# Kernel tuning notes

Measured on AMD Instinct MI355X. Metric: run time of the kernel, lower is better.

Reference implementation:

```python
import jax, jax.numpy as jnp
import numpy as np

D = 1024  # input_dim


def setup_inputs() -> dict:
    key = jax.random.key(0)
    ks = jax.random.split(key, 7)
    scale = 1.0 / np.sqrt(D)
    x = jax.random.normal(ks[0], (4, D, 2048), dtype=jnp.float32)
    Wq = jax.random.uniform(ks[1], (D, D), jnp.float32, -scale, scale)
    bq = jax.random.uniform(ks[2], (D,), jnp.float32, -scale, scale)
    Wk = jax.random.uniform(ks[3], (D, D), jnp.float32, -scale, scale)
    bk = jax.random.uniform(ks[4], (D,), jnp.float32, -scale, scale)
    Wv = jax.random.uniform(ks[5], (D, D), jnp.float32, -scale, scale)
    bv = jax.random.uniform(ks[6], (D,), jnp.float32, -scale, scale)
    return {"x": x, "Wq": Wq, "bq": bq, "Wk": Wk, "bk": bk, "Wv": Wv, "bv": bv}


def reference(x, Wq, bq, Wk, bk, Wv, bv):
    # x: [B, D, S] -> [B, S, D]
    xt = jnp.transpose(x, (0, 2, 1))
    # torch nn.Linear: y = x @ W^T + b
    q = jnp.einsum('bsd,ed->bse', xt, Wq) + bq
    k = jnp.einsum('bsd,ed->bse', xt, Wk) + bk
    v = jnp.einsum('bsd,ed->bse', xt, Wv) + bv
    scores = jnp.einsum('bse,bte->bst', q, k) / jnp.sqrt(jnp.float32(D))
    attn = jax.nn.softmax(scores, axis=2)
    out = jnp.einsum('bst,bte->bse', attn, v)  # [B, S, D]
    return out
```

## Files before the change

### kernel.cpp

```cpp
#include <hip/hip_runtime.h>
#include <stdint.h>

typedef unsigned short us16;
typedef unsigned short us8  __attribute__((ext_vector_type(8)));
typedef unsigned short us4v __attribute__((ext_vector_type(4)));
typedef __bf16         bf16x8 __attribute__((ext_vector_type(8)));
typedef float          f32x4  __attribute__((ext_vector_type(4)));

__device__ __forceinline__ us16 f2bf(float f) {
    union { float f; unsigned int u; } c; c.f = f;
    unsigned int u = (c.u + 0x7fffu + ((c.u >> 16) & 1u)) >> 16;
    return (us16)u;
}

__device__ __forceinline__ void async16(const us16* g, us16* l) {
    __builtin_amdgcn_global_load_lds(
        (const __attribute__((address_space(1))) unsigned int*)g,
        (__attribute__((address_space(3))) unsigned int*)l,
        16, 0, 0);
}

template <int N> __device__ __forceinline__ void wait_vm() {
    if constexpr (N == 8)      asm volatile("s_waitcnt vmcnt(8)" ::: "memory");
    else if constexpr (N == 6) asm volatile("s_waitcnt vmcnt(6)" ::: "memory");
    else if constexpr (N == 4) asm volatile("s_waitcnt vmcnt(4)" ::: "memory");
    else if constexpr (N == 3) asm volatile("s_waitcnt vmcnt(3)" ::: "memory");
    else                       asm volatile("s_waitcnt vmcnt(0)" ::: "memory");
}

template <int EPI, int MI, int NJ>
__device__ __forceinline__ void gemm_pipe(
        const us16* __restrict__ A, const us16* __restrict__ B,
        void* __restrict__ C, const float* __restrict__ bias,
        float* __restrict__ L,
        int M, int K, int x, int y, us16* lds) {
    constexpr int BM  = 32 * MI;
    constexpr int BN  = 64 * NJ;
    constexpr int IA  = BM / 128;
    constexpr int IB  = BN / 128;
    constexpr int EA  = BM * 32;
    constexpr int BUF = EA + BN * 32;
    constexpr int LD  = IA + IB;

    const int tid  = threadIdx.x;
    const int lane = tid & 63, wid = tid >> 6;
    const int l15  = lane & 15, quad = lane >> 4;
    const int wm   = wid >> 2, wn = wid & 3;
    const int m0   = x * BM, n0 = y * BN;

    const int gc8  = (((lane & 3) ^ ((lane >> 2) & 3) ^ ((lane >> 4) & 3))) * 8;
    const int lsub = lane >> 2;

    const us16* Ag[IA]; int Al[IA];
#pragma unroll
    for (int c = 0; c < IA; c++) {
        const int r = wid * (16 * IA) + c * 16;
        Ag[c] = A + (size_t)(m0 + r + lsub) * K + gc8;
        Al[c] = r * 32;
    }
    const us16* Bg[IB]; int Bl[IB];
#pragma unroll
    for (int c = 0; c < IB; c++) {
        const int r = wid * (16 * IB) + c * 16;
        Bg[c] = B + (size_t)(n0 + r + lsub) * K + gc8;
        Bl[c] = EA + r * 32;
    }

    const int NT  = K >> 5;
    const int rc8    = ((quad ^ (l15 & 3) ^ ((l15 >> 2) & 3))) * 8;
    const int raBase = wm * (MI * 16) + l15;
    const int rbBase = wn * (NJ * 16) + l15;

    f32x4 acc[MI][NJ] = {};

#pragma unroll
    for (int t = 0; t < 3; t++) {
        us16* bp = lds + t * BUF;
        const int ko = t * 32;
#pragma unroll
        for (int c = 0; c < IA; c++) async16(Ag[c] + ko, bp + Al[c]);
#pragma unroll
        for (int c = 0; c < IB; c++) async16(Bg[c] + ko, bp + Bl[c]);
    }
    wait_vm<2 * LD>();
    __builtin_amdgcn_s_barrier();

    for (int t = 0; t < NT; t++) {
        if (t + 3 < NT) {
            us16* bp = lds + ((t + 3) & 3) * BUF;
            const int ko = (t + 3) * 32;
#pragma unroll
            for (int c = 0; c < IA; c++) async16(Ag[c] + ko, bp + Al[c]);
#pragma unroll
            for (int c = 0; c < IB; c++) async16(Bg[c] + ko, bp + Bl[c]);
        }
        const us16* bp = lds + (t & 3) * BUF;
        bf16x8 af[MI], bfv[NJ];
#pragma unroll
        for (int i = 0; i < MI; i++)
            af[i]  = *(const bf16x8*)(bp + (raBase + i * 16) * 32 + rc8);
#pragma unroll
        for (int j = 0; j < NJ; j++)
            bfv[j] = *(const bf16x8*)(bp + EA + (rbBase + j * 16) * 32 + rc8);
        __builtin_amdgcn_s_setprio(1);
#pragma unroll
        for (int i = 0; i < MI; i++)
#pragma unroll
            for (int j = 0; j < NJ; j++)
                acc[i][j] = __builtin_amdgcn_mfma_f32_16x16x32_bf16(af[i], bfv[j], acc[i][j], 0, 0, 0);
        __builtin_amdgcn_s_setprio(0);
        if (t + 3 < NT)      wait_vm<2 * LD>();
        else if (t + 2 < NT) wait_vm<LD>();
        else if (t + 1 < NT) wait_vm<0>();
        __builtin_amdgcn_sched_barrier(0);
        __builtin_amdgcn_s_barrier();
    }

    if (EPI == 2) {
        const float scale = 0.03125f;
        float rs[NJ];
#pragma unroll
        for (int j = 0; j < NJ; j++) rs[j] = 0.f;
#pragma unroll
        for (int i = 0; i < MI; i++) {
            const int mb = m0 + wm * (MI * 16) + i * 16 + quad * 4;
#pragma unroll
            for (int j = 0; j < NJ; j++) {
                const int n = n0 + wn * (NJ * 16) + j * 16 + l15;
                f32x4 v = acc[i][j];
                const float e0 = __expf(v[0] * scale), e1 = __expf(v[1] * scale);
                const float e2 = __expf(v[2] * scale), e3 = __expf(v[3] * scale);
                rs[j] += (e0 + e1) + (e2 + e3);
                us4v st = { f2bf(e0), f2bf(e1), f2bf(e2), f2bf(e3) };
                *(us4v*)((us16*)C + (size_t)n * M + mb) = st;
            }
        }
#pragma unroll
        for (int j = 0; j < NJ; j++) {
            rs[j] += __shfl_xor(rs[j], 16, 64);
            rs[j] += __shfl_xor(rs[j], 32, 64);
        }
        if (quad == 0) {
#pragma unroll
            for (int j = 0; j < NJ; j++)
                atomicAdd(&L[n0 + wn * (NJ * 16) + j * 16 + l15], rs[j]);
        }
        return;
    }

#pragma unroll
    for (int i = 0; i < MI; i++) {
        const int mb = m0 + wm * (MI * 16) + i * 16 + quad * 4;
        float b0 = 0.f, b1 = 0.f, b2 = 0.f, b3 = 0.f;
        if (EPI == 0) {
            float4 bv4 = *(const float4*)(bias + mb);
            b0 = bv4.x; b1 = bv4.y; b2 = bv4.z; b3 = bv4.w;
        }
#pragma unroll
        for (int j = 0; j < NJ; j++) {
            const int n = n0 + wn * (NJ * 16) + j * 16 + l15;
            f32x4 v = acc[i][j];
            if (EPI == 3) {
                const float inv = 1.0f / L[n];
                float4 st;
                st.x = v[0] * inv; st.y = v[1] * inv;
                st.z = v[2] * inv; st.w = v[3] * inv;
                *(float4*)((float*)C + (size_t)n * M + mb) = st;
            } else {
                const float bn = (EPI == 1) ? bias[n] : 0.0f;
                us4v st = { f2bf(v[0] + b0 + bn), f2bf(v[1] + b1 + bn),
                            f2bf(v[2] + b2 + bn), f2bf(v[3] + b3 + bn) };
                *(us4v*)((us16*)C + (size_t)n * M + mb) = st;
            }
        }
    }
}

__device__ __forceinline__ void strip_xy(int lin, int gy, int& x, int& y) {
    const int within = lin & (4 * gy - 1);
    x = (lin / (4 * gy)) * 4 + (within & 3);
    y = within >> 2;
}

__global__ __launch_bounds__(256)
void prep(const float* __restrict__ x, us16* __restrict__ xt,
          const float* __restrict__ wq, const float* __restrict__ wk,
          const float* __restrict__ wv, us16* __restrict__ wb) {
    __shared__ us16 tile[64 * 65];
    const int id = blockIdx.x;
    const int t = threadIdx.x;
    if (id < 2048) {
        const int s0 = (id & 31) * 64, d0 = ((id >> 5) & 15) * 64, b = id >> 9;
        const float* xp = x + ((size_t)b * 1024 + d0) * 2048 + s0;
        const int r = t >> 4, c4 = t & 15;
#pragma unroll
        for (int i = 0; i < 4; i++) {
            float4 v = *(const float4*)(xp + (size_t)(r + 16 * i) * 2048 + c4 * 4);
            const int d = r + 16 * i;
            tile[(c4 * 4 + 0) * 65 + d] = f2bf(v.x);
            tile[(c4 * 4 + 1) * 65 + d] = f2bf(v.y);
            tile[(c4 * 4 + 2) * 65 + d] = f2bf(v.z);
            tile[(c4 * 4 + 3) * 65 + d] = f2bf(v.w);
        }
        __syncthreads();
        us16* op = xt + ((size_t)b * 2048 + s0) * 1024 + d0;
#pragma unroll
        for (int i = 0; i < 2; i++) {
            const int u = t + 256 * i;
            const int s = u >> 3, c8 = u & 7;
            us8 o;
#pragma unroll
            for (int j = 0; j < 8; j++) o[j] = tile[s * 65 + c8 * 8 + j];
            *(us8*)(op + (size_t)s * 1024 + c8 * 8) = o;
        }
    } else {
        const int cid = id - 2048;
        const int mb = cid >> 10;
        const float* src = (mb == 0) ? wq : (mb == 1) ? wk : wv;
        const size_t off = ((size_t)(cid & 1023) * 256 + t) * 4;
        float4 v = *(const float4*)(src + off);
        us4v o = { f2bf(v.x), f2bf(v.y), f2bf(v.z), f2bf(v.w) };
        *(us4v*)(wb + (size_t)mb * 1048576 + off) = o;
    }
}

__global__ __launch_bounds__(512)
void qkv(const us16* __restrict__ Wb, const us16* __restrict__ XT,
         us16* __restrict__ Qb, us16* __restrict__ Kb, us16* __restrict__ VT,
         const float* __restrict__ bq, const float* __restrict__ bk,
         const float* __restrict__ bv) {
    __shared__ __align__(16) us16 lds[65536];
    const int id = blockIdx.x;
    const long long sXT = 2097152;
    if (id < 256) {
        const int z = id >> 5, zz = z & 3;
        const bool isK = z >= 4;
        int x, y; strip_xy(id & 31, 8, x, y);
        const us16* A = Wb + (isK ? 1048576 : 0);
        const us16* B = XT + (size_t)zz * sXT;
        us16* C = (isK ? Kb : Qb) + (size_t)zz * sXT;
        gemm_pipe<0, 8, 4>(A, B, (void*)C, isK ? bk : bq, nullptr,
                           1024, 1024, x, y, lds);
    } else {
        const int id2 = id - 256;
        const int z = id2 >> 6;
        int x, y; strip_xy(id2 & 63, 4, x, y);
        gemm_pipe<1, 4, 4>(XT + (size_t)z * sXT, Wb + 2097152,
                           (void*)(VT + (size_t)z * sXT), bv, nullptr,
                           2048, 1024, x, y, lds);
    }
}

__global__ __launch_bounds__(512)
void scores_k(const us16* __restrict__ Kb, const us16* __restrict__ Qb,
              us16* __restrict__ Sb, float* __restrict__ L) {
    __shared__ __align__(16) us16 lds[65536];
    const long long sXT = 2097152, sSS = 4194304;
    const int z = blockIdx.z;
    int x, y; strip_xy(blockIdx.x + 8 * blockIdx.y, 8, x, y);
    gemm_pipe<2, 8, 4>(Kb + (size_t)z * sXT, Qb + (size_t)z * sXT,
                       (void*)(Sb + (size_t)z * sSS), nullptr, L + z * 2048,
                       2048, 1024, x, y, lds);
}

__global__ __launch_bounds__(512)
void out_k(const us16* __restrict__ VT, const us16* __restrict__ Sb,
           float* __restrict__ L, float* __restrict__ out) {
    __shared__ __align__(16) us16 lds[49152];
    const long long sXT = 2097152, sSS = 4194304;
    const int z = blockIdx.z;
    int x, y; strip_xy(blockIdx.x + 8 * blockIdx.y, 8, x, y);
    gemm_pipe<3, 4, 4>(VT + (size_t)z * sXT, Sb + (size_t)z * sSS,
                       (void*)(out + (size_t)z * sXT), nullptr, L + z * 2048,
                       1024, 2048, x, y, lds);
}

extern "C" void kernel_launch(void* const* d_in, const int* in_sizes, int n_in,
                              void* d_out, int out_size, void* d_ws, size_t ws_size,
                              hipStream_t stream) {
    const float* x  = (const float*)d_in[0];
    const float* Wq = (const float*)d_in[1];
    const float* bq = (const float*)d_in[2];
    const float* Wk = (const float*)d_in[3];
    const float* bk = (const float*)d_in[4];
    const float* Wv = (const float*)d_in[5];
    const float* bv = (const float*)d_in[6];
    float* out = (float*)d_out;
    char* ws = (char*)d_ws;

    const size_t SZ = 16777216;
    us16* Qb = (us16*)(ws);
    us16* Kb = (us16*)(ws + SZ);
    us16* VT = (us16*)(ws + 2 * SZ);
    us16* XT = (us16*)(ws + 3 * SZ);
    us16* Wb = (us16*)(ws + 4 * SZ);
    us16* Sb = (us16*)(ws + 3 * SZ);
    float* Lb = (float*)(ws + 5 * SZ);

    hipMemsetAsync(Lb, 0, 4 * 2048 * sizeof(float), stream);
    prep<<<dim3(5120, 1, 1), dim3(256, 1, 1), 0, stream>>>(x, XT, Wq, Wk, Wv, Wb);
    qkv<<<dim3(512, 1, 1), dim3(512, 1, 1), 0, stream>>>(Wb, XT, Qb, Kb, VT, bq, bk, bv);
    scores_k<<<dim3(8, 8, 4), dim3(512, 1, 1), 0, stream>>>(Kb, Qb, Sb, Lb);
    out_k<<<dim3(8, 8, 4), dim3(512, 1, 1), 0, stream>>>(VT, Sb, Lb, out);
}
```

Measured before the change: 244.5 us.

## Rework GEMM mainloop to double-buffered BK=64 tiles with phased MFMA barriers

Replaces the four-stage, BK=32 async LDS pipeline with a two-stage, BK=64 double buffer using a new XOR swizzle over 64-element rows. Each K step now loads B fragments once and splits the A fragments and MFMAs into four phases separated by workgroup barriers. The goal is fewer loop iterations and fewer barriers per unit of K, plus more MFMA work per LDS read. In exchange the prefetch depth drops from three tiles to one, and the extra per-phase barriers may expose memory latency.

```diff
diff --git a/kernel.cpp b/kernel.cpp
--- a/kernel.cpp
+++ b/kernel.cpp
@@ -23,110 +23,102 @@
 template <int N> __device__ __forceinline__ void wait_vm() {
     if constexpr (N == 8)      asm volatile("s_waitcnt vmcnt(8)" ::: "memory");
     else if constexpr (N == 6) asm volatile("s_waitcnt vmcnt(6)" ::: "memory");
-    else if constexpr (N == 4) asm volatile("s_waitcnt vmcnt(4)" ::: "memory");
-    else if constexpr (N == 3) asm volatile("s_waitcnt vmcnt(3)" ::: "memory");
     else                       asm volatile("s_waitcnt vmcnt(0)" ::: "memory");
 }
 
-template <int EPI, int MI, int NJ>
-__device__ __forceinline__ void gemm_pipe(
+template <int EPI, int MI>
+__device__ __forceinline__ void gemm_core(
         const us16* __restrict__ A, const us16* __restrict__ B,
         void* __restrict__ C, const float* __restrict__ bias,
         float* __restrict__ L,
         int M, int K, int x, int y, us16* lds) {
-    constexpr int BM  = 32 * MI;
-    constexpr int BN  = 64 * NJ;
-    constexpr int IA  = BM / 128;
-    constexpr int IB  = BN / 128;
-    constexpr int EA  = BM * 32;
-    constexpr int BUF = EA + BN * 32;
-    constexpr int LD  = IA + IB;
+    constexpr int BM     = MI * 32;
+    constexpr int BOFF   = BM * 64;
+    constexpr int BUF    = (BM + 256) * 64;
+    constexpr int ACALLS = BM / 64;
+    constexpr int NVM    = ACALLS + 4;
+    constexpr int PMI    = MI / 4;
 
     const int tid  = threadIdx.x;
     const int lane = tid & 63, wid = tid >> 6;
     const int l15  = lane & 15, quad = lane >> 4;
     const int wm   = wid >> 2, wn = wid & 3;
-    const int m0   = x * BM, n0 = y * BN;
-
-    const int gc8  = (((lane & 3) ^ ((lane >> 2) & 3) ^ ((lane >> 4) & 3))) * 8;
-    const int lsub = lane >> 2;
-
-    const us16* Ag[IA]; int Al[IA];
-#pragma unroll
-    for (int c = 0; c < IA; c++) {
-        const int r = wid * (16 * IA) + c * 16;
-        Ag[c] = A + (size_t)(m0 + r + lsub) * K + gc8;
-        Al[c] = r * 32;
-    }
-    const us16* Bg[IB]; int Bl[IB];
-#pragma unroll
-    for (int c = 0; c < IB; c++) {
-        const int r = wid * (16 * IB) + c * 16;
-        Bg[c] = B + (size_t)(n0 + r + lsub) * K + gc8;
-        Bl[c] = EA + r * 32;
-    }
-
-    const int NT  = K >> 5;
-    const int rc8    = ((quad ^ (l15 & 3) ^ ((l15 >> 2) & 3))) * 8;
-    const int raBase = wm * (MI * 16) + l15;
-    const int rbBase = wn * (NJ * 16) + l15;
-
-    f32x4 acc[MI][NJ] = {};
-
-#pragma unroll
-    for (int t = 0; t < 3; t++) {
-        us16* bp = lds + t * BUF;
-        const int ko = t * 32;
-#pragma unroll
-        for (int c = 0; c < IA; c++) async16(Ag[c] + ko, bp + Al[c]);
-#pragma unroll
-        for (int c = 0; c < IB; c++) async16(Bg[c] + ko, bp + Bl[c]);
-    }
-    wait_vm<2 * LD>();
-    __builtin_amdgcn_s_barrier();
+    const int m0   = x * BM, n0 = y * 256;
+
+    const int srow = tid >> 3;
+    const int sc   = ((tid & 7) ^ (srow & 7)) * 8;
+    const us16* Ag = A + (size_t)(m0 + srow) * K + sc;
+    const us16* Bg = B + (size_t)(n0 + srow) * K + sc;
+    const int sl   = tid * 8;
+
+    f32x4 acc[MI][4] = {};
+    const int NT = K >> 6;
+
+#pragma unroll
+    for (int c = 0; c < ACALLS; c++) async16(Ag + (size_t)(c * 64) * K, lds + c * 4096 + sl);
+#pragma unroll
+    for (int c = 0; c < 4; c++)      async16(Bg + (size_t)(c * 64) * K, lds + BOFF + c * 4096 + sl);
 
     for (int t = 0; t < NT; t++) {
-        if (t + 3 < NT) {
-            us16* bp = lds + ((t + 3) & 3) * BUF;
-            const int ko = (t + 3) * 32;
-#pragma unroll
-            for (int c = 0; c < IA; c++) async16(Ag[c] + ko, bp + Al[c]);
-#pragma unroll
-            for (int c = 0; c < IB; c++) async16(Bg[c] + ko, bp + Bl[c]);
-        }
-        const us16* bp = lds + (t & 3) * BUF;
-        bf16x8 af[MI], bfv[NJ];
-#pragma unroll
-        for (int i = 0; i < MI; i++)
-            af[i]  = *(const bf16x8*)(bp + (raBase + i * 16) * 32 + rc8);
-#pragma unroll
-        for (int j = 0; j < NJ; j++)
-            bfv[j] = *(const bf16x8*)(bp + EA + (rbBase + j * 16) * 32 + rc8);
-        __builtin_amdgcn_s_setprio(1);
-#pragma unroll
-        for (int i = 0; i < MI; i++)
-#pragma unroll
-            for (int j = 0; j < NJ; j++)
-                acc[i][j] = __builtin_amdgcn_mfma_f32_16x16x32_bf16(af[i], bfv[j], acc[i][j], 0, 0, 0);
-        __builtin_amdgcn_s_setprio(0);
-        if (t + 3 < NT)      wait_vm<2 * LD>();
-        else if (t + 2 < NT) wait_vm<LD>();
-        else if (t + 1 < NT) wait_vm<0>();
+        const us16* cur = lds + (t & 1) * BUF;
+        if (t + 1 < NT) {
+            us16* nxt = lds + ((t + 1) & 1) * BUF;
+            const size_t ko = (size_t)(t + 1) * 64;
+#pragma unroll
+            for (int c = 0; c < ACALLS; c++) async16(Ag + (size_t)(c * 64) * K + ko, nxt + c * 4096 + sl);
+#pragma unroll
+            for (int c = 0; c < 4; c++)      async16(Bg + (size_t)(c * 64) * K + ko, nxt + BOFF + c * 4096 + sl);
+            wait_vm<NVM>();
+        } else {
+            wait_vm<0>();
+        }
         __builtin_amdgcn_sched_barrier(0);
         __builtin_amdgcn_s_barrier();
+        __builtin_amdgcn_sched_barrier(0);
+
+        bf16x8 bf[4][2];
+#pragma unroll
+        for (int nj = 0; nj < 4; nj++) {
+            const int rb = wn * 64 + nj * 16 + l15;
+#pragma unroll
+            for (int ks = 0; ks < 2; ks++)
+                bf[nj][ks] = *(const bf16x8*)(cur + BOFF + rb * 64 + ((ks * 4 + quad) ^ (rb & 7)) * 8);
+        }
+#pragma unroll
+        for (int p = 0; p < 4; p++) {
+            bf16x8 af[PMI][2];
+#pragma unroll
+            for (int i = 0; i < PMI; i++) {
+                const int ra = wm * (MI * 16) + (p * PMI + i) * 16 + l15;
+#pragma unroll
+                for (int ks = 0; ks < 2; ks++)
+                    af[i][ks] = *(const bf16x8*)(cur + ra * 64 + ((ks * 4 + quad) ^ (ra & 7)) * 8);
+            }
+            __builtin_amdgcn_s_setprio(1);
+#pragma unroll
+            for (int ks = 0; ks < 2; ks++)
+#pragma unroll
+                for (int i = 0; i < PMI; i++)
+#pragma unroll
+                    for (int nj = 0; nj < 4; nj++)
+                        acc[p * PMI + i][nj] = __builtin_amdgcn_mfma_f32_16x16x32_bf16(
+                            af[i][ks], bf[nj][ks], acc[p * PMI + i][nj], 0, 0, 0);
+            __builtin_amdgcn_s_setprio(0);
+            __builtin_amdgcn_sched_barrier(0);
+            __builtin_amdgcn_s_barrier();
+            __builtin_amdgcn_sched_barrier(0);
+        }
     }
 
     if (EPI == 2) {
         const float scale = 0.03125f;
-        float rs[NJ];
-#pragma unroll
-        for (int j = 0; j < NJ; j++) rs[j] = 0.f;
+        float rs[4] = {0.f, 0.f, 0.f, 0.f};
 #pragma unroll
         for (int i = 0; i < MI; i++) {
             const int mb = m0 + wm * (MI * 16) + i * 16 + quad * 4;
 #pragma unroll
-            for (int j = 0; j < NJ; j++) {
-                const int n = n0 + wn * (NJ * 16) + j * 16 + l15;
+            for (int j = 0; j < 4; j++) {
+                const int n = n0 + wn * 64 + j * 16 + l15;
                 f32x4 v = acc[i][j];
                 const float e0 = __expf(v[0] * scale), e1 = __expf(v[1] * scale);
                 const float e2 = __expf(v[2] * scale), e3 = __expf(v[3] * scale);
@@ -136,14 +128,14 @@
             }
         }
 #pragma unroll
-        for (int j = 0; j < NJ; j++) {
+        for (int j = 0; j < 4; j++) {
             rs[j] += __shfl_xor(rs[j], 16, 64);
             rs[j] += __shfl_xor(rs[j], 32, 64);
         }
         if (quad == 0) {
 #pragma unroll
-            for (int j = 0; j < NJ; j++)
-                atomicAdd(&L[n0 + wn * (NJ * 16) + j * 16 + l15], rs[j]);
+            for (int j = 0; j < 4; j++)
+                atomicAdd(&L[n0 + wn * 64 + j * 16 + l15], rs[j]);
         }
         return;
     }
@@ -157,8 +149,8 @@
             b0 = bv4.x; b1 = bv4.y; b2 = bv4.z; b3 = bv4.w;
         }
 #pragma unroll
-        for (int j = 0; j < NJ; j++) {
-            const int n = n0 + wn * (NJ * 16) + j * 16 + l15;
+        for (int j = 0; j < 4; j++) {
+            const int n = n0 + wn * 64 + j * 16 + l15;
             f32x4 v = acc[i][j];
             if (EPI == 3) {
                 const float inv = 1.0f / L[n];
@@ -239,15 +231,14 @@
         const us16* A = Wb + (isK ? 1048576 : 0);
         const us16* B = XT + (size_t)zz * sXT;
         us16* C = (isK ? Kb : Qb) + (size_t)zz * sXT;
-        gemm_pipe<0, 8, 4>(A, B, (void*)C, isK ? bk : bq, nullptr,
-                           1024, 1024, x, y, lds);
+        gemm_core<0, 8>(A, B, (void*)C, isK ? bk : bq, nullptr, 1024, 1024, x, y, lds);
     } else {
         const int id2 = id - 256;
         const int z = id2 >> 6;
         int x, y; strip_xy(id2 & 63, 4, x, y);
-        gemm_pipe<1, 4, 4>(XT + (size_t)z * sXT, Wb + 2097152,
-                           (void*)(VT + (size_t)z * sXT), bv, nullptr,
-                           2048, 1024, x, y, lds);
+        gemm_core<1, 4>(XT + (size_t)z * sXT, Wb + 2097152,
+                        (void*)(VT + (size_t)z * sXT), bv, nullptr,
+                        2048, 1024, x, y, lds);
     }
 }
 
@@ -258,9 +249,9 @@
     const long long sXT = 2097152, sSS = 4194304;
     const int z = blockIdx.z;
     int x, y; strip_xy(blockIdx.x + 8 * blockIdx.y, 8, x, y);
-    gemm_pipe<2, 8, 4>(Kb + (size_t)z * sXT, Qb + (size_t)z * sXT,
-                       (void*)(Sb + (size_t)z * sSS), nullptr, L + z * 2048,
-                       2048, 1024, x, y, lds);
+    gemm_core<2, 8>(Kb + (size_t)z * sXT, Qb + (size_t)z * sXT,
+                    (void*)(Sb + (size_t)z * sSS), nullptr, L + z * 2048,
+                    2048, 1024, x, y, lds);
 }
 
 __global__ __launch_bounds__(512)
@@ -270,9 +261,9 @@
     const long long sXT = 2097152, sSS = 4194304;
     const int z = blockIdx.z;
     int x, y; strip_xy(blockIdx.x + 8 * blockIdx.y, 8, x, y);
-    gemm_pipe<3, 4, 4>(VT + (size_t)z * sXT, Sb + (size_t)z * sSS,
-                       (void*)(out + (size_t)z * sXT), nullptr, L + z * 2048,
-                       1024, 2048, x, y, lds);
+    gemm_core<3, 4>(VT + (size_t)z * sXT, Sb + (size_t)z * sSS,
+                    (void*)(out + (size_t)z * sXT), nullptr, L + z * 2048,
+                    1024, 2048, x, y, lds);
 }
 
 extern "C" void kernel_launch(void* const* d_in, const int* in_sizes, int n_in,
```

Result: no change. 239.9 us (-1.9%).
